# Kernel tuning notes

Measured on AMD Instinct MI355X. Metric: run time of the kernel, lower is better.

Reference implementation:

```python
import jax, jax.numpy as jnp
import numpy as np

B, L, D = 4, 2048, 1024
H, DK, DV = 16, 64, 64


def setup_inputs() -> dict:
    key = jax.random.key(0)
    ks = jax.random.split(key, 11)
    s = 1.0 / np.sqrt(D)
    so = 1.0 / np.sqrt(H * DV)
    return {
        "query": jax.random.normal(ks[0], (B, L, D), jnp.float32),
        "key": jax.random.normal(ks[1], (B, L, D), jnp.float32),
        "value": jax.random.normal(ks[2], (B, L, D), jnp.float32),
        "W_q": jax.random.uniform(ks[3], (D, H * DK), jnp.float32, -s, s),
        "b_q": jax.random.uniform(ks[4], (H * DK,), jnp.float32, -s, s),
        "W_k": jax.random.uniform(ks[5], (D, H * DK), jnp.float32, -s, s),
        "b_k": jax.random.uniform(ks[6], (H * DK,), jnp.float32, -s, s),
        "W_v": jax.random.uniform(ks[7], (D, H * DV), jnp.float32, -s, s),
        "b_v": jax.random.uniform(ks[8], (H * DV,), jnp.float32, -s, s),
        "W_o": jax.random.uniform(ks[9], (H * DV, D), jnp.float32, -so, so),
        "b_o": jax.random.uniform(ks[10], (D,), jnp.float32, -so, so),
    }


def reference(query, key, value, W_q, b_q, W_k, b_k, W_v, b_v, W_o, b_o):
    # QKV projections, then split heads: [B, L, H*d] -> [B, H, L, d]
    q = (query @ W_q + b_q).reshape(B, L, H, DK).transpose(0, 2, 1, 3)
    k = (key @ W_k + b_k).reshape(B, L, H, DK).transpose(0, 2, 1, 3)
    v = (value @ W_v + b_v).reshape(B, L, H, DV).transpose(0, 2, 1, 3)
    # scaled dot-product attention: softmax(q k^T / sqrt(dk)) v
    scores = jnp.einsum("bhqd,bhkd->bhqk", q, k) / jnp.sqrt(jnp.float32(DK))
    attn = jax.nn.softmax(scores, axis=-1)
    ctx = jnp.einsum("bhqk,bhkd->bhqd", attn, v)
    # combine heads: [B, H, L, dv] -> [B, L, H*dv], output projection
    out = ctx.transpose(0, 2, 1, 3).reshape(B, L, H * DV) @ W_o + b_o
    return out
```

## Files before the change

kernel.cpp:

```cpp
#include <hip/hip_runtime.h>

#define BATCH 4
#define LSEQ 2048
#define DMODEL 1024
#define NHEAD 16
#define DHEAD 64
#define MTOT (BATCH * LSEQ)

typedef _Float16 f16;
typedef _Float16 f16x8 __attribute__((ext_vector_type(8)));
typedef _Float16 f16x4 __attribute__((ext_vector_type(4)));
typedef float f32x4 __attribute__((ext_vector_type(4)));

#define SCORE_SCALE 0.180336878f

typedef const __attribute__((address_space(1))) void gvoid;
typedef __attribute__((address_space(3))) void lvoid;
#define GLDS16(g, l) __builtin_amdgcn_global_load_lds((gvoid*)(g), (lvoid*)(l), 16, 0, 0)

__global__ __launch_bounds__(256)
void cvt3_f32_f16(const float* __restrict__ in0, const float* __restrict__ in1,
                  const float* __restrict__ in2, f16* __restrict__ out, int n8)
{
    const int y = blockIdx.y;
    const float* in = (y == 0) ? in0 : (y == 1) ? in1 : in2;
    f16* o = out + (size_t)y * (size_t)n8 * 8;
    int i = blockIdx.x * 256 + threadIdx.x;
    if (i >= n8) return;
    float4 a = ((const float4*)in)[2 * i];
    float4 b = ((const float4*)in)[2 * i + 1];
    f16x8 v;
    v[0] = (f16)a.x; v[1] = (f16)a.y; v[2] = (f16)a.z; v[3] = (f16)a.w;
    v[4] = (f16)b.x; v[5] = (f16)b.y; v[6] = (f16)b.z; v[7] = (f16)b.w;
    ((f16x8*)o)[i] = v;
}

__global__ __launch_bounds__(256)
void wconv4(const float* __restrict__ W0, const float* __restrict__ W1,
            const float* __restrict__ W2, const float* __restrict__ W3,
            f16* __restrict__ WtBase)
{
    __shared__ float T[64][68];
    const int z = blockIdx.z;
    const float* W = (z == 0) ? W0 : (z == 1) ? W1 : (z == 2) ? W2 : W3;
    f16* Wt = WtBase + (size_t)z * DMODEL * DMODEL;
    const int t = threadIdx.x;
    const int k0 = blockIdx.y * 64, n0 = blockIdx.x * 64;
    const int tr = t >> 4, tc = (t & 15) * 4;
#pragma unroll
    for (int p = 0; p < 64; p += 16) {
        float4 v = *(const float4*)&W[(size_t)(k0 + tr + p) * DMODEL + n0 + tc];
        *(float4*)&T[tr + p][tc] = v;
    }
    __syncthreads();
    const int n = t >> 2, kc = (t & 3) * 16;
    f16x8 o0, o1;
#pragma unroll
    for (int j = 0; j < 8; ++j) o0[j] = (f16)T[kc + j][n];
#pragma unroll
    for (int j = 0; j < 8; ++j) o1[j] = (f16)T[kc + 8 + j][n];
    *(f16x8*)&Wt[(size_t)(n0 + n) * DMODEL + k0 + kc] = o0;
    *(f16x8*)&Wt[(size_t)(n0 + n) * DMODEL + k0 + kc + 8] = o1;
}

__global__ __launch_bounds__(256)
void gemm_f16(const f16* __restrict__ A, const f16* __restrict__ Bt,
              const float* __restrict__ b0, const float* __restrict__ b1,
              const float* __restrict__ b2, void* __restrict__ Cout, int fused)
{
    __shared__ f16 As2[2][128][32];
    __shared__ f16 Bs2[2][128][32];

    const int t = threadIdx.x;
    const int lane = t & 63, w = t >> 6;
    const int quad = lane >> 4, m16 = lane & 15;
    const int m0 = blockIdx.x * 128;
    const int n0 = blockIdx.y * 128;
    const int wm = (w & 1) * 64, wn = (w >> 1) * 64;

    const int which = fused ? (n0 >> 10) : 0;

    f32x4 acc[4][4] = {};

    const f16* Ag = A + (size_t)which * MTOT * DMODEL
                      + (size_t)(m0 + (t >> 2)) * DMODEL + (t & 3) * 8;
    const f16* Bg = Bt + (size_t)(n0 + (t >> 2)) * DMODEL + (t & 3) * 8;
    f16* Al = &As2[0][0][0] + t * 8;
    f16* Bl = &Bs2[0][0][0] + t * 8;

    for (int k0 = 0; k0 < DMODEL; k0 += 64) {
        __syncthreads();
#pragma unroll
        for (int h = 0; h < 2; ++h) {
            GLDS16(Ag + k0 + h * 32, Al + h * 4096);
            GLDS16(Ag + k0 + h * 32 + (size_t)64 * DMODEL, Al + h * 4096 + 2048);
            GLDS16(Bg + k0 + h * 32, Bl + h * 4096);
            GLDS16(Bg + k0 + h * 32 + (size_t)64 * DMODEL, Bl + h * 4096 + 2048);
        }
        __syncthreads();
#pragma unroll
        for (int h = 0; h < 2; ++h) {
            f16x8 af[4], bf[4];
#pragma unroll
            for (int mi = 0; mi < 4; ++mi)
                af[mi] = *(const f16x8*)&As2[h][wm + mi * 16 + m16][quad * 8];
#pragma unroll
            for (int ni = 0; ni < 4; ++ni)
                bf[ni] = *(const f16x8*)&Bs2[h][wn + ni * 16 + m16][quad * 8];
#pragma unroll
            for (int mi = 0; mi < 4; ++mi)
#pragma unroll
                for (int ni = 0; ni < 4; ++ni)
                    acc[mi][ni] = __builtin_amdgcn_mfma_f32_16x16x32_f16(
                        af[mi], bf[ni], acc[mi][ni], 0, 0, 0);
        }
    }

    if (fused) {
        const float* bp = (which == 0) ? b0 : (which == 1) ? b1 : b2;
        const float scale = (which == 0) ? SCORE_SCALE : 1.0f;
        f16* o = (f16*)Cout + (size_t)which * MTOT * DMODEL;
#pragma unroll
        for (int ni = 0; ni < 4; ++ni) {
            const int nn = (n0 + wn + ni * 16 + m16) & 1023;
            const float bv = bp[nn];
            const int h = nn >> 6, d = nn & 63;
#pragma unroll
            for (int mi = 0; mi < 4; ++mi) {
                const int mrow = m0 + wm + mi * 16 + quad * 4;
                const int b = mrow >> 11, l0 = mrow & (LSEQ - 1);
                if (which < 2) {
#pragma unroll
                    for (int j = 0; j < 4; ++j) {
                        const float v = (acc[mi][ni][j] + bv) * scale;
                        o[(((size_t)(b * NHEAD + h) * LSEQ + l0 + j) << 6) + d] = (f16)v;
                    }
                } else {
                    f16x4 pk;
#pragma unroll
                    for (int j = 0; j < 4; ++j) pk[j] = (f16)(acc[mi][ni][j] + bv);
                    *(f16x4*)&o[(((size_t)(b * NHEAD + h) << 6) + d) * LSEQ + l0] = pk;
                }
            }
        }
    } else {
#pragma unroll
        for (int ni = 0; ni < 4; ++ni) {
            const int n = n0 + wn + ni * 16 + m16;
            const float bv = b0[n];
#pragma unroll
            for (int mi = 0; mi < 4; ++mi)
#pragma unroll
                for (int j = 0; j < 4; ++j) {
                    const int m = m0 + wm + mi * 16 + quad * 4 + j;
                    ((float*)Cout)[(size_t)m * DMODEL + n] = acc[mi][ni][j] + bv;
                }
        }
    }
}

__global__ __launch_bounds__(256, 2)
void attn_mfma(const f16* __restrict__ Qh, const f16* __restrict__ Kh,
               const f16* __restrict__ Vt, f16* __restrict__ ctx)
{
    __shared__ f16 Ks[2][64][32];
    __shared__ f16 Vs[2][64][32];
    __shared__ f16 Ps[256][72];

    const int t = threadIdx.x;
    const int lane = t & 63, w = t >> 6;
    const int quad = lane >> 4, m16 = lane & 15;

    const int bid = blockIdx.x;
    const int x = bid & 7, rest = bid >> 3;
    const int qt = rest & 7;
    const int g = x + 8 * (rest >> 3);
    const int q0 = qt * 256, wq = w * 64;

    const f16* Qg = Qh + (size_t)g * LSEQ * DHEAD;
    const f16* Kg = Kh + (size_t)g * LSEQ * DHEAD;
    const f16* Vg = Vt + (size_t)g * LSEQ * DHEAD;

    f16x8 qa[4][2];
#pragma unroll
    for (int qi = 0; qi < 4; ++qi)
#pragma unroll
        for (int ks = 0; ks < 2; ++ks)
            qa[qi][ks] = *(const f16x8*)&Qg[(size_t)(q0 + wq + qi * 16 + m16) * DHEAD
                                            + ks * 32 + quad * 8];

    f32x4 ctxa[4][4] = {};
    float lsum[4] = {0.f, 0.f, 0.f, 0.f};

    const f16* ksrc = Kg + (size_t)(t >> 2) * DHEAD + (t & 3) * 8;
    const f16* vsrc = Vg + (size_t)(t >> 2) * LSEQ + (t & 3) * 8;
    f16* kdst = &Ks[0][0][0] + t * 8;
    f16* vdst = &Vs[0][0][0] + t * 8;

    for (int kt = 0; kt < LSEQ; kt += 64) {
        __syncthreads();
        GLDS16(ksrc + (size_t)kt * DHEAD, kdst);
        GLDS16(ksrc + (size_t)kt * DHEAD + 32, kdst + 2048);
        GLDS16(vsrc + kt, vdst);
        GLDS16(vsrc + kt + 32, vdst + 2048);
        __syncthreads();

        f16x8 kb[4][2];
#pragma unroll
        for (int ki = 0; ki < 4; ++ki)
#pragma unroll
            for (int ks = 0; ks < 2; ++ks)
                kb[ki][ks] = *(const f16x8*)&Ks[ks][ki * 16 + m16][quad * 8];

        f32x4 s[4][4];
#pragma unroll
        for (int ki = 0; ki < 4; ++ki)
#pragma unroll
            for (int qi = 0; qi < 4; ++qi) {
                f32x4 z = {0.f, 0.f, 0.f, 0.f};
                z = __builtin_amdgcn_mfma_f32_16x16x32_f16(kb[ki][0], qa[qi][0], z, 0, 0, 0);
                s[ki][qi] = __builtin_amdgcn_mfma_f32_16x16x32_f16(kb[ki][1], qa[qi][1], z, 0, 0, 0);
            }

#pragma unroll
        for (int ki = 0; ki < 4; ++ki)
#pragma unroll
            for (int qi = 0; qi < 4; ++qi) {
                f16x4 pk;
#pragma unroll
                for (int j = 0; j < 4; ++j) {
                    const float p = __builtin_amdgcn_exp2f(s[ki][qi][j]);
                    lsum[qi] += p;
                    pk[j] = (f16)p;
                }
                *(f16x4*)&Ps[wq + qi * 16 + m16][ki * 16 + quad * 4] = pk;
            }

        f16x8 pa[4][2], vb[4][2];
#pragma unroll
        for (int qi = 0; qi < 4; ++qi)
#pragma unroll
            for (int ks = 0; ks < 2; ++ks)
                pa[qi][ks] = *(const f16x8*)&Ps[wq + qi * 16 + m16][ks * 32 + quad * 8];
#pragma unroll
        for (int di = 0; di < 4; ++di)
#pragma unroll
            for (int ks = 0; ks < 2; ++ks)
                vb[di][ks] = *(const f16x8*)&Vs[ks][di * 16 + m16][quad * 8];
#pragma unroll
        for (int qi = 0; qi < 4; ++qi)
#pragma unroll
            for (int di = 0; di < 4; ++di) {
                ctxa[qi][di] = __builtin_amdgcn_mfma_f32_16x16x32_f16(pa[qi][0], vb[di][0], ctxa[qi][di], 0, 0, 0);
                ctxa[qi][di] = __builtin_amdgcn_mfma_f32_16x16x32_f16(pa[qi][1], vb[di][1], ctxa[qi][di], 0, 0, 0);
            }
    }

    float linv[4];
#pragma unroll
    for (int qi = 0; qi < 4; ++qi) {
        float l = lsum[qi];
        l += __shfl_xor(l, 16);
        l += __shfl_xor(l, 32);
        linv[qi] = 1.0f / l;
    }

    const int batch = g >> 4, h = g & 15;
#pragma unroll
    for (int qi = 0; qi < 4; ++qi)
#pragma unroll
        for (int j = 0; j < 4; ++j) {
            const float inv = __shfl(linv[qi], quad * 4 + j);
            const int l = q0 + wq + qi * 16 + quad * 4 + j;
#pragma unroll
            for (int di = 0; di < 4; ++di) {
                const int col = h * 64 + di * 16 + m16;
                ctx[((size_t)batch * LSEQ + l) * DMODEL + col] = (f16)(ctxa[qi][di][j] * inv);
            }
        }
}

extern "C" void kernel_launch(void* const* d_in, const int* in_sizes, int n_in,
                              void* d_out, int out_size, void* d_ws, size_t ws_size,
                              hipStream_t stream)
{
    const float* query = (const float*)d_in[0];
    const float* key   = (const float*)d_in[1];
    const float* value = (const float*)d_in[2];
    const float* W_q   = (const float*)d_in[3];
    const float* b_q   = (const float*)d_in[4];
    const float* W_k   = (const float*)d_in[5];
    const float* b_k   = (const float*)d_in[6];
    const float* W_v   = (const float*)d_in[7];
    const float* b_v   = (const float*)d_in[8];
    const float* W_o   = (const float*)d_in[9];
    const float* b_o   = (const float*)d_in[10];
    float* out = (float*)d_out;

    const size_t MAT = (size_t)MTOT * DMODEL;
    f16* base = (f16*)d_ws;
    f16* Aq   = base;
    f16* Qhp  = base + 3 * MAT;
    f16* ctxh = base + 6 * MAT;
    f16* Wtq  = base + 7 * MAT;
    f16* Wto  = Wtq + (size_t)3 * DMODEL * DMODEL;

    const int n8 = (int)(MAT / 8);
    cvt3_f32_f16<<<dim3(n8 / 256, 3), 256, 0, stream>>>(query, key, value, Aq, n8);
    wconv4<<<dim3(DMODEL / 64, DMODEL / 64, 4), 256, 0, stream>>>(W_q, W_k, W_v, W_o, Wtq);

    gemm_f16<<<dim3(MTOT / 128, 3 * DMODEL / 128), 256, 0, stream>>>(
        Aq, Wtq, b_q, b_k, b_v, Qhp, 1);

    attn_mfma<<<BATCH * NHEAD * (LSEQ / 256), 256, 0, stream>>>(
        Qhp, Qhp + MAT, Qhp + 2 * MAT, ctxh);

    gemm_f16<<<dim3(MTOT / 128, DMODEL / 128), 256, 0, stream>>>(
        ctxh, Wto, b_o, nullptr, nullptr, out, 0);
}
```

Measured before the change: 340.9 us.

## Restructure attention kernel with 32x32 MFMA, register-resident P and double-buffered K/V

Rewrites the attention kernel to use 32x32x16 MFMA tiles, with 8 waves per block each owning 32 query rows. The probability tile stays in registers, rearranged with a cross-half lane shuffle, instead of going through a shared-memory P buffer. K/V tiles are stored in XOR-swizzled LDS and double-buffered so the next tile's global-to-LDS load overlaps compute. The aim is to cut LDS traffic and bank conflicts and hide load latency, at the cost of more complex lane shuffles and higher register pressure under the 512-thread launch bound.

```diff
diff --git a/kernel.cpp b/kernel.cpp
--- a/kernel.cpp
+++ b/kernel.cpp
@@ -10,7 +10,11 @@
 typedef _Float16 f16;
 typedef _Float16 f16x8 __attribute__((ext_vector_type(8)));
 typedef _Float16 f16x4 __attribute__((ext_vector_type(4)));
+typedef _Float16 f16x2 __attribute__((ext_vector_type(2)));
 typedef float f32x4 __attribute__((ext_vector_type(4)));
+typedef float f32x16 __attribute__((ext_vector_type(16)));
+typedef unsigned int u32;
+typedef unsigned int u32x4 __attribute__((ext_vector_type(4)));
 
 #define SCORE_SCALE 0.180336878f
 
@@ -159,125 +163,126 @@
     }
 }
 
-__global__ __launch_bounds__(256, 2)
+__global__ __launch_bounds__(512, 4)
 void attn_mfma(const f16* __restrict__ Qh, const f16* __restrict__ Kh,
                const f16* __restrict__ Vt, f16* __restrict__ ctx)
 {
-    __shared__ f16 Ks[2][64][32];
-    __shared__ f16 Vs[2][64][32];
-    __shared__ f16 Ps[256][72];
+    __shared__ f16 Ks[2][64 * 64];
+    __shared__ f16 Vs[2][64 * 64];
 
     const int t = threadIdx.x;
     const int lane = t & 63, w = t >> 6;
-    const int quad = lane >> 4, m16 = lane & 15;
+    const int l31 = lane & 31;
+    const int hi = lane >> 5;
+    const int swz = (l31 & 7) << 4;
 
     const int bid = blockIdx.x;
     const int x = bid & 7, rest = bid >> 3;
     const int qt = rest & 7;
     const int g = x + 8 * (rest >> 3);
-    const int q0 = qt * 256, wq = w * 64;
+    const int q0 = qt * 256 + w * 32;
 
     const f16* Qg = Qh + (size_t)g * LSEQ * DHEAD;
     const f16* Kg = Kh + (size_t)g * LSEQ * DHEAD;
     const f16* Vg = Vt + (size_t)g * LSEQ * DHEAD;
 
-    f16x8 qa[4][2];
-#pragma unroll
-    for (int qi = 0; qi < 4; ++qi)
-#pragma unroll
-        for (int ks = 0; ks < 2; ++ks)
-            qa[qi][ks] = *(const f16x8*)&Qg[(size_t)(q0 + wq + qi * 16 + m16) * DHEAD
-                                            + ks * 32 + quad * 8];
-
-    f32x4 ctxa[4][4] = {};
-    float lsum[4] = {0.f, 0.f, 0.f, 0.f};
-
-    const f16* ksrc = Kg + (size_t)(t >> 2) * DHEAD + (t & 3) * 8;
-    const f16* vsrc = Vg + (size_t)(t >> 2) * LSEQ + (t & 3) * 8;
-    f16* kdst = &Ks[0][0][0] + t * 8;
-    f16* vdst = &Vs[0][0][0] + t * 8;
-
-    for (int kt = 0; kt < LSEQ; kt += 64) {
+    f16x8 qf[4];
+#pragma unroll
+    for (int s = 0; s < 4; ++s)
+        qf[s] = *(const f16x8*)&Qg[(size_t)(q0 + l31) * DHEAD + 16 * s + 8 * hi];
+
+    const int srow = t >> 3;
+    const int sxs = ((t & 7) << 4) ^ ((srow & 7) << 4);
+    const f16* ksrc = Kg + (size_t)srow * DHEAD + (sxs >> 1);
+    const f16* vsrc = Vg + (size_t)srow * LSEQ + (sxs >> 1);
+    f16* kdst0 = &Ks[0][0] + t * 8;
+    f16* vdst0 = &Vs[0][0] + t * 8;
+    f16* kdst1 = &Ks[1][0] + t * 8;
+    f16* vdst1 = &Vs[1][0] + t * 8;
+
+    f32x16 ctxa[2] = {};
+    float lsum = 0.f;
+
+    GLDS16(ksrc, kdst0);
+    GLDS16(vsrc, vdst0);
+    __syncthreads();
+
+    auto proc = [&](const f32x16& stv, const int kb, const char* Vc) {
+        u32 d[8];
+#pragma unroll
+        for (int r = 0; r < 8; ++r) {
+            const float p0 = __builtin_amdgcn_exp2f(stv[2 * r]);
+            const float p1 = __builtin_amdgcn_exp2f(stv[2 * r + 1]);
+            lsum += p0 + p1;
+            f16x2 pk; pk[0] = (f16)p0; pk[1] = (f16)p1;
+            d[r] = __builtin_bit_cast(u32, pk);
+        }
+#pragma unroll
+        for (int s = 0; s < 2; ++s) {
+            const u32 sendE = hi ? d[4 * s + 0] : d[4 * s + 2];
+            const u32 sendO = hi ? d[4 * s + 1] : d[4 * s + 3];
+            const u32 recvE = __shfl_xor(sendE, 32);
+            const u32 recvO = __shfl_xor(sendO, 32);
+            u32x4 paw;
+            paw[0] = hi ? recvE : d[4 * s + 0];
+            paw[1] = hi ? recvO : d[4 * s + 1];
+            paw[2] = hi ? d[4 * s + 2] : recvE;
+            paw[3] = hi ? d[4 * s + 3] : recvO;
+            const f16x8 pa = __builtin_bit_cast(f16x8, paw);
+            const int kbyte = kb * 64 + 32 * s + 16 * hi;
+#pragma unroll
+            for (int d32 = 0; d32 < 2; ++d32) {
+                const int vrow = d32 * 32 + l31;
+                const f16x8 vf = *(const f16x8*)(Vc + vrow * 128 + (kbyte ^ swz));
+                ctxa[d32] = __builtin_amdgcn_mfma_f32_32x32x16_f16(
+                    pa, vf, ctxa[d32], 0, 0, 0);
+            }
+        }
+    };
+
+    auto compute = [&](const f16* Kbuf, const f16* Vbuf) {
+        const char* Kc = (const char*)Kbuf;
+        const char* Vc = (const char*)Vbuf;
+        f32x16 s0 = {}, s1 = {};
+#pragma unroll
+        for (int s = 0; s < 4; ++s) {
+            const int cb = 32 * s + 16 * hi;
+            const f16x8 kf0 = *(const f16x8*)(Kc + l31 * 128 + (cb ^ swz));
+            const f16x8 kf1 = *(const f16x8*)(Kc + (l31 + 32) * 128 + (cb ^ swz));
+            s0 = __builtin_amdgcn_mfma_f32_32x32x16_f16(kf0, qf[s], s0, 0, 0, 0);
+            s1 = __builtin_amdgcn_mfma_f32_32x32x16_f16(kf1, qf[s], s1, 0, 0, 0);
+        }
+        proc(s0, 0, Vc);
+        proc(s1, 1, Vc);
+    };
+
+    for (int kt = 0; kt < LSEQ; kt += 128) {
+        if (kt + 64 < LSEQ) {
+            GLDS16(ksrc + (size_t)(kt + 64) * DHEAD, kdst1);
+            GLDS16(vsrc + (kt + 64), vdst1);
+        }
+        compute(&Ks[0][0], &Vs[0][0]);
         __syncthreads();
-        GLDS16(ksrc + (size_t)kt * DHEAD, kdst);
-        GLDS16(ksrc + (size_t)kt * DHEAD + 32, kdst + 2048);
-        GLDS16(vsrc + kt, vdst);
-        GLDS16(vsrc + kt + 32, vdst + 2048);
+        if (kt + 128 < LSEQ) {
+            GLDS16(ksrc + (size_t)(kt + 128) * DHEAD, kdst0);
+            GLDS16(vsrc + (kt + 128), vdst0);
+        }
+        compute(&Ks[1][0], &Vs[1][0]);
         __syncthreads();
-
-        f16x8 kb[4][2];
-#pragma unroll
-        for (int ki = 0; ki < 4; ++ki)
-#pragma unroll
-            for (int ks = 0; ks < 2; ++ks)
-                kb[ki][ks] = *(const f16x8*)&Ks[ks][ki * 16 + m16][quad * 8];
-
-        f32x4 s[4][4];
-#pragma unroll
-        for (int ki = 0; ki < 4; ++ki)
-#pragma unroll
-            for (int qi = 0; qi < 4; ++qi) {
-                f32x4 z = {0.f, 0.f, 0.f, 0.f};
-                z = __builtin_amdgcn_mfma_f32_16x16x32_f16(kb[ki][0], qa[qi][0], z, 0, 0, 0);
-                s[ki][qi] = __builtin_amdgcn_mfma_f32_16x16x32_f16(kb[ki][1], qa[qi][1], z, 0, 0, 0);
-            }
-
-#pragma unroll
-        for (int ki = 0; ki < 4; ++ki)
-#pragma unroll
-            for (int qi = 0; qi < 4; ++qi) {
-                f16x4 pk;
-#pragma unroll
-                for (int j = 0; j < 4; ++j) {
-                    const float p = __builtin_amdgcn_exp2f(s[ki][qi][j]);
-                    lsum[qi] += p;
-                    pk[j] = (f16)p;
-                }
-                *(f16x4*)&Ps[wq + qi * 16 + m16][ki * 16 + quad * 4] = pk;
-            }
-
-        f16x8 pa[4][2], vb[4][2];
-#pragma unroll
-        for (int qi = 0; qi < 4; ++qi)
-#pragma unroll
-            for (int ks = 0; ks < 2; ++ks)
-                pa[qi][ks] = *(const f16x8*)&Ps[wq + qi * 16 + m16][ks * 32 + quad * 8];
-#pragma unroll
-        for (int di = 0; di < 4; ++di)
-#pragma unroll
-            for (int ks = 0; ks < 2; ++ks)
-                vb[di][ks] = *(const f16x8*)&Vs[ks][di * 16 + m16][quad * 8];
-#pragma unroll
-        for (int qi = 0; qi < 4; ++qi)
-#pragma unroll
-            for (int di = 0; di < 4; ++di) {
-                ctxa[qi][di] = __builtin_amdgcn_mfma_f32_16x16x32_f16(pa[qi][0], vb[di][0], ctxa[qi][di], 0, 0, 0);
-                ctxa[qi][di] = __builtin_amdgcn_mfma_f32_16x16x32_f16(pa[qi][1], vb[di][1], ctxa[qi][di], 0, 0, 0);
-            }
-    }
-
-    float linv[4];
-#pragma unroll
-    for (int qi = 0; qi < 4; ++qi) {
-        float l = lsum[qi];
-        l += __shfl_xor(l, 16);
-        l += __shfl_xor(l, 32);
-        linv[qi] = 1.0f / l;
-    }
-
+    }
+
+    const float l = lsum + __shfl_xor(lsum, 32);
+    const float linv = 1.0f / l;
     const int batch = g >> 4, h = g & 15;
 #pragma unroll
-    for (int qi = 0; qi < 4; ++qi)
-#pragma unroll
-        for (int j = 0; j < 4; ++j) {
-            const float inv = __shfl(linv[qi], quad * 4 + j);
-            const int l = q0 + wq + qi * 16 + quad * 4 + j;
-#pragma unroll
-            for (int di = 0; di < 4; ++di) {
-                const int col = h * 64 + di * 16 + m16;
-                ctx[((size_t)batch * LSEQ + l) * DMODEL + col] = (f16)(ctxa[qi][di][j] * inv);
-            }
-        }
+    for (int r = 0; r < 16; ++r) {
+        const int qr = (r & 3) + 8 * (r >> 2) + 4 * hi;
+        const float inv = __shfl(linv, qr);
+        f16* op = ctx + ((size_t)(batch * LSEQ + q0 + qr)) * DMODEL
+                      + h * 64 + l31;
+        op[0]  = (f16)(ctxa[0][r] * inv);
+        op[32] = (f16)(ctxa[1][r] * inv);
+    }
 }
 
 extern "C" void kernel_launch(void* const* d_in, const int* in_sizes, int n_in,
@@ -312,7 +317,7 @@
     gemm_f16<<<dim3(MTOT / 128, 3 * DMODEL / 128), 256, 0, stream>>>(
         Aq, Wtq, b_q, b_k, b_v, Qhp, 1);
 
-    attn_mfma<<<BATCH * NHEAD * (LSEQ / 256), 256, 0, stream>>>(
+    attn_mfma<<<BATCH * NHEAD * (LSEQ / 256), 512, 0, stream>>>(
         Qhp, Qhp + MAT, Qhp + 2 * MAT, ctxh);
 
     gemm_f16<<<dim3(MTOT / 128, DMODEL / 128), 256, 0, stream>>>(
```

New measurement: 337.8 us. About the same (-0.9%).
